# Kernel tuning notes

Measured on AMD Instinct MI355X. Metric: run time of the kernel, lower is better.

## Reference

```python
import jax, jax.numpy as jnp
import numpy as np

N = 100000          # buses
E = 200000          # branch edges (avg degree 2, power grid)
IN_DIM = 6          # x[:, 4:10]
EDGE_DIM = 4
HID = 32
OUT_DIM = 2


def _nnconv(x_in, src, dst, edge_attr, w1, b1, w2, b2, root, bias):
    """PyG NNConv (aggr='add', root_weight=True, bias=True)."""
    in_c, out_c = root.shape
    # edge-conditioned weight matrices: [E, in_c, out_c]
    h = jax.nn.relu(edge_attr @ w1 + b1)
    W = (h @ w2 + b2).reshape(-1, in_c, out_c)
    # gather source features, per-edge matvec, scatter-add to targets
    msg = jnp.einsum('ei,eio->eo', x_in[src], W)           # [E, out_c]
    agg = jax.ops.segment_sum(msg, dst, num_segments=x_in.shape[0])
    return agg + x_in @ root + bias


def setup_inputs() -> dict:
    key = jax.random.key(0)
    ks = jax.random.split(key, 8)
    inp = {
        'x': jax.random.normal(ks[0], (N, 10), dtype=jnp.float32),
        'edge_index': jax.random.randint(ks[1], (2, E), 0, N, dtype=jnp.int64),
        'edge_attr': jax.random.normal(ks[2], (E, EDGE_DIM), dtype=jnp.float32),
    }
    dims = [(IN_DIM, HID), (HID, HID), (HID, HID), (HID, OUT_DIM)]
    s = 0.1
    for i, (ic, oc) in enumerate(dims):
        k = jax.random.split(ks[3 + i], 3)
        inp[f'w1_{i}'] = jax.random.normal(k[0], (EDGE_DIM, HID), dtype=jnp.float32) * s
        inp[f'b1_{i}'] = jnp.zeros((HID,), dtype=jnp.float32)
        inp[f'w2_{i}'] = jax.random.normal(k[1], (HID, ic * oc), dtype=jnp.float32) * s
        inp[f'b2_{i}'] = jnp.zeros((ic * oc,), dtype=jnp.float32)
        inp[f'root_{i}'] = jax.random.normal(k[2], (ic, oc), dtype=jnp.float32) * s
        inp[f'bias_{i}'] = jnp.zeros((oc,), dtype=jnp.float32)
    return inp


def reference(x, edge_index, edge_attr,
              w1_0, b1_0, w2_0, b2_0, root_0, bias_0,
              w1_1, b1_1, w2_1, b2_1, root_1, bias_1,
              w1_2, b1_2, w2_2, b2_2, root_2, bias_2,
              w1_3, b1_3, w2_3, b2_3, root_3, bias_3):
    convs = [
        (w1_0, b1_0, w2_0, b2_0, root_0, bias_0),
        (w1_1, b1_1, w2_1, b2_1, root_1, bias_1),
        (w1_2, b1_2, w2_2, b2_2, root_2, bias_2),
        (w1_3, b1_3, w2_3, b2_3, root_3, bias_3),
    ]
    src, dst = edge_index[0], edge_index[1]
    h = x[:, 4:10]                                    # [N, 6]
    n_convs = len(convs)
    for i, p in enumerate(convs):
        h = _nnconv(h, src, dst, edge_attr, *p)
        if i < n_convs - 1:
            h = jax.nn.relu(h)
    return h
```

## Files before the change

### kernel.cpp

```cpp
#include <hip/hip_runtime.h>
#include <hip/hip_fp16.h>

typedef __attribute__((ext_vector_type(2)))  _Float16 half2v;
typedef __attribute__((ext_vector_type(8)))  _Float16 half8v;
typedef __attribute__((ext_vector_type(16))) float    f32x16;

static constexpr int BSWZ_STEPS = 226;
static constexpr int BSWZ_TOT   = BSWZ_STEPS * 512;
static constexpr int W1H_TOT    = 4 * 160;

struct Prm {
    const float* x;
    const float* w1[4]; const float* b1[4];
    const float* w2[4]; const float* b2[4];
    const float* root[4]; const float* bias[4];
    _Float16* xin;
    _Float16* bswz;
    _Float16* w1h;
    _Float16* aggz;
    float* outz;
    int N;
};

__global__ __launch_bounds__(256) void prep(Prm p, int NB8, int NZA, int NZO)
{
    int b = blockIdx.x;
    if (b < 452) {
        int i = b * 256 + threadIdx.x;
        int T = i >> 9, t2 = i & 511;
        int j = t2 & 7, l = (t2 >> 3) & 63;
        int g = l >> 5, o = l & 31;
        int layer, cls, t;
        if (T < 17)       { layer = 0; cls = 0; t = T; }
        else if (T < 19)  { layer = 0; cls = 1; t = T - 17; }
        else if (T < 85)  { layer = 1; cls = 0; t = T - 19; }
        else if (T < 88)  { layer = 1; cls = 1; t = T - 85; }
        else if (T < 154) { layer = 2; cls = 0; t = T - 88; }
        else if (T < 157) { layer = 2; cls = 1; t = T - 154; }
        else if (T < 223) { layer = 3; cls = 0; t = T - 157; }
        else              { layer = 3; cls = 1; t = T - 223; }
        const int INP   = (layer == 0) ? 8 : 32;
        const int IN_C  = (layer == 0) ? 6 : 32;
        const int OUT_C = (layer == 3) ? 2 : 32;
        float v = 0.f;
        if (cls == 0) {
            const int S_MAIN = 2 * INP;
            if (t < S_MAIN) {
                int kap = 16 * t + 8 * g + j;
                int k  = (INP == 8) ? (kap >> 3) : (kap >> 5);
                int ii = (INP == 8) ? (kap & 7)  : (kap & 31);
                if (ii < IN_C && o < OUT_C)
                    v = p.w2[layer][(size_t)k * (IN_C * OUT_C) + ii * OUT_C + o];
            } else {
                int ii = 16 * (t - S_MAIN) + 8 * g + j;
                if (ii < IN_C && o < OUT_C)
                    v = p.b2[layer][ii * OUT_C + o];
            }
        } else {
            const int nroot = (layer == 0) ? 1 : 2;
            if (t < nroot) {
                int ii = 16 * t + 8 * g + j;
                if (ii < IN_C && o < OUT_C)
                    v = p.root[layer][ii * OUT_C + o];
            } else {
                if (g == 0 && j == 0 && o < OUT_C)
                    v = p.bias[layer][o];
            }
        }
        p.bswz[i] = (_Float16)v;
    } else if (b < 452 + NB8) {
        int i = (b - 452) * 256 + threadIdx.x;
        if (i < p.N * 8) {
            int v = i >> 3, c = i & 7;
            float val = (c < 6) ? p.x[(size_t)v * 10 + 4 + c] : 0.f;
            p.xin[i] = (_Float16)val;
        }
    } else if (b < 452 + NB8 + NZA) {
        long long i = (long long)(b - 452 - NB8) * 256 + threadIdx.x;
        if (i < (long long)p.N * 12)
            ((uint4*)p.aggz)[i] = uint4{0u, 0u, 0u, 0u};
    } else if (b < 452 + NB8 + NZA + NZO) {
        int v = (b - 452 - NB8 - NZA) * 256 + threadIdx.x;
        if (v < p.N)
            ((float2*)p.outz)[v] = float2{0.f, 0.f};
    } else {
        for (int i = threadIdx.x; i < W1H_TOT; i += 256) {
            int layer = i / 160, r = i % 160;
            float v = (r < 128) ? p.w1[layer][r]
                                : p.b1[layer][r - 128];
            p.w1h[i] = (_Float16)v;
        }
    }
}

static __device__ __forceinline__ void gather32h(
    const _Float16* __restrict__ fprev, int s, int g, half8v& xh0, half8v& xh1)
{
    const half8v* fp = (const half8v*)(fprev + (size_t)s * 32);
    xh0 = fp[g];
    xh1 = fp[2 + g];
    #pragma unroll
    for (int j = 0; j < 8; ++j) {
        xh0[j] = xh0[j] > (_Float16)0.f ? xh0[j] : (_Float16)0.f;
        xh1[j] = xh1[j] > (_Float16)0.f ? xh1[j] : (_Float16)0.f;
    }
}

static __device__ __forceinline__ half8v splat8(_Float16 h)
{
    half8v r;
    #pragma unroll
    for (int j = 0; j < 8; ++j) r[j] = h;
    return r;
}

static __device__ __forceinline__ void pk_atomic_row(
    _Float16* __restrict__ aggH, int row, int o, float mine)
{
    float oth = __shfl_xor(mine, 1);
    if ((o & 1) == 0 && row >= 0) {
        __half2 v = __floats2half2_rn(mine, oth);
        unsafeAtomicAdd((__half2*)aggH + (((size_t)row << 5) + o) / 2, v);
    }
}

template<int INP, int OUT_C>
__global__ __launch_bounds__(1024, 8) void edge(
    const _Float16* __restrict__ xin,
    const _Float16* __restrict__ fprev,
    const int*      __restrict__ src,
    const int*      __restrict__ dst,
    const float*    __restrict__ ea,
    const _Float16* __restrict__ w1h,
    const _Float16* __restrict__ bAll,
    _Float16* __restrict__ aggH,
    float*    __restrict__ aggF,
    int E, int N, int ntileE, int ntot)
{
    constexpr int NREAL = (INP == 32) ? 66 : 17;
    constexpr int NSELF = (INP == 32) ? 3  : 2;
    constexpr int NSTEP = NREAL + NSELF;

    __shared__ half8v ldsb[NSTEP * 64];
    {
        const half8v* bp = (const half8v*)bAll;
        for (int i = threadIdx.x; i < NSTEP * 64; i += 1024)
            ldsb[i] = bp[i];
    }
    __syncthreads();

    const int lane = threadIdx.x & 63;
    const int g = lane >> 5, o = lane & 31;
    const int lrow = lane & 31;
    const int wv = (blockIdx.x * 1024 + threadIdx.x) >> 6;
    const int nw = gridDim.x * 16;

    const half2v* w1p = (const half2v*)w1h;
    const half2v* b1p = (const half2v*)(w1h + 128);
    const half2v zero2 = { (_Float16)0.f, (_Float16)0.f };

    half8v ones;
    #pragma unroll
    for (int j = 0; j < 8; ++j) ones[j] = (_Float16)0.f;
    ones[0] = (_Float16)1.f;

    for (int tile = wv; tile < ntot; tile += nw) {
        f32x16 C;
        #pragma unroll
        for (int i = 0; i < 16; ++i) C[i] = 0.f;

        if (tile < ntileE) {
            const int e0 = tile * 32;
            const int er = e0 + lrow;
            const int ec = er < E ? er : (E - 1);
            const int s  = src[ec];
            const float4 av = *(const float4*)(ea + 4ll * ec);
            half2v eax; eax[0] = (_Float16)av.x; eax[1] = eax[0];
            half2v eay; eay[0] = (_Float16)av.y; eay[1] = eay[0];
            half2v eaz; eaz[0] = (_Float16)av.z; eaz[1] = eaz[0];
            half2v eaw; eaw[0] = (_Float16)av.w; eaw[1] = eaw[0];

            half8v xh0, xh1;
            if constexpr (INP == 32) gather32h(fprev, s, g, xh0, xh1);
            else                     xh0 = *(const half8v*)(xin + (size_t)s * 8);

            if constexpr (INP == 32) {
                #pragma unroll 2
                for (int t = 0; t < 16; ++t) {
                    half2v h2 = eax * w1p[t] + b1p[t];
                    h2 = eay * w1p[16 + t] + h2;
                    h2 = eaz * w1p[32 + t] + h2;
                    h2 = eaw * w1p[48 + t] + h2;
                    h2 = __builtin_elementwise_max(h2, zero2);
                    half8v hsl = splat8(h2[0]);
                    half8v hsh = splat8(h2[1]);
                    half8v bf0 = ldsb[(4*t    ) * 64 + lane];
                    half8v bf1 = ldsb[(4*t + 1) * 64 + lane];
                    half8v bf2 = ldsb[(4*t + 2) * 64 + lane];
                    half8v bf3 = ldsb[(4*t + 3) * 64 + lane];
                    C = __builtin_amdgcn_mfma_f32_32x32x16_f16(hsl * xh0, bf0, C, 0, 0, 0);
                    C = __builtin_amdgcn_mfma_f32_32x32x16_f16(hsl * xh1, bf1, C, 0, 0, 0);
                    C = __builtin_amdgcn_mfma_f32_32x32x16_f16(hsh * xh0, bf2, C, 0, 0, 0);
                    C = __builtin_amdgcn_mfma_f32_32x32x16_f16(hsh * xh1, bf3, C, 0, 0, 0);
                }
                C = __builtin_amdgcn_mfma_f32_32x32x16_f16(xh0, ldsb[64*64 + lane], C, 0, 0, 0);
                C = __builtin_amdgcn_mfma_f32_32x32x16_f16(xh1, ldsb[65*64 + lane], C, 0, 0, 0);
            } else {
                #pragma unroll 4
                for (int t = 0; t < 16; ++t) {
                    half2v h2 = eax * w1p[t] + b1p[t];
                    h2 = eay * w1p[16 + t] + h2;
                    h2 = eaz * w1p[32 + t] + h2;
                    h2 = eaw * w1p[48 + t] + h2;
                    h2 = __builtin_elementwise_max(h2, zero2);
                    half8v hs = splat8(g ? h2[1] : h2[0]);
                    half8v bf = ldsb[t * 64 + lane];
                    C = __builtin_amdgcn_mfma_f32_32x32x16_f16(hs * xh0, bf, C, 0, 0, 0);
                }
                half8v zz;
                #pragma unroll
                for (int j = 0; j < 8; ++j) zz[j] = (_Float16)0.f;
                half8v a = (g == 0) ? xh0 : zz;
                C = __builtin_amdgcn_mfma_f32_32x32x16_f16(a, ldsb[16*64 + lane], C, 0, 0, 0);
            }

            if constexpr (OUT_C == 32) {
                #pragma unroll
                for (int q = 0; q < 4; ++q) {
                    const int eb = e0 + 8 * q + 4 * g;
                    int rows[4];
                    if (eb + 3 < E) {
                        const int4 dd = *(const int4*)(dst + eb);
                        rows[0] = dd.x; rows[1] = dd.y; rows[2] = dd.z; rows[3] = dd.w;
                    } else {
                        #pragma unroll
                        for (int m = 0; m < 4; ++m)
                            rows[m] = (eb + m < E) ? dst[eb + m] : -1;
                    }
                    #pragma unroll
                    for (int m = 0; m < 4; ++m)
                        pk_atomic_row(aggH, rows[m], o, C[4*q + m]);
                }
            } else {
                if (o < OUT_C) {
                    #pragma unroll
                    for (int q = 0; q < 4; ++q) {
                        const int eb = e0 + 8 * q + 4 * g;
                        #pragma unroll
                        for (int m = 0; m < 4; ++m)
                            if (eb + m < E)
                                unsafeAtomicAdd(aggF + (size_t)dst[eb + m] * OUT_C + o,
                                                C[4*q + m]);
                    }
                }
            }
        } else {
            const int v0 = (tile - ntileE) * 32;
            const int vr = v0 + lrow;
            const int vc = vr < N ? vr : (N - 1);

            if constexpr (INP == 32) {
                half8v xh0, xh1;
                gather32h(fprev, vc, g, xh0, xh1);
                C = __builtin_amdgcn_mfma_f32_32x32x16_f16(xh0,  ldsb[(NREAL+0)*64 + lane], C, 0, 0, 0);
                C = __builtin_amdgcn_mfma_f32_32x32x16_f16(xh1,  ldsb[(NREAL+1)*64 + lane], C, 0, 0, 0);
                C = __builtin_amdgcn_mfma_f32_32x32x16_f16(ones, ldsb[(NREAL+2)*64 + lane], C, 0, 0, 0);
            } else {
                half8v xh0 = *(const half8v*)(xin + (size_t)vc * 8);
                C = __builtin_amdgcn_mfma_f32_32x32x16_f16(xh0,  ldsb[(NREAL+0)*64 + lane], C, 0, 0, 0);
                C = __builtin_amdgcn_mfma_f32_32x32x16_f16(ones, ldsb[(NREAL+1)*64 + lane], C, 0, 0, 0);
            }

            if constexpr (OUT_C == 32) {
                #pragma unroll
                for (int q = 0; q < 4; ++q) {
                    #pragma unroll
                    for (int m = 0; m < 4; ++m) {
                        const int row = v0 + 8*q + 4*g + m;
                        pk_atomic_row(aggH, row < N ? row : -1, o, C[4*q + m]);
                    }
                }
            } else {
                if (o < OUT_C) {
                    #pragma unroll
                    for (int q = 0; q < 4; ++q) {
                        #pragma unroll
                        for (int m = 0; m < 4; ++m) {
                            const int row = v0 + 8*q + 4*g + m;
                            if (row < N)
                                unsafeAtomicAdd(aggF + (size_t)row * OUT_C + o, C[4*q + m]);
                        }
                    }
                }
            }
        }
    }
}

extern "C" void kernel_launch(void* const* d_in, const int* in_sizes, int n_in,
                              void* d_out, int out_size, void* d_ws, size_t ws_size,
                              hipStream_t stream)
{
    const float* x  = (const float*)d_in[0];
    const int*   ei = (const int*)d_in[1];
    const float* ea = (const float*)d_in[2];

    const int E = in_sizes[2] / 4;
    const int N = in_sizes[0] / 10;
    const int* src = ei;
    const int* dst = ei + E;

    const float* p[4][6];
    for (int L = 0; L < 4; ++L)
        for (int j = 0; j < 6; ++j)
            p[L][j] = (const float*)d_in[3 + 6 * L + j];

    char* w = (char*)d_ws;
    auto carve = [&](size_t bytes) {
        char* q = w; w += (bytes + 255) & ~(size_t)255; return (void*)q;
    };
    _Float16* xin  = (_Float16*)carve((size_t)N * 8 * 2);
    _Float16* aggz = (_Float16*)carve((size_t)3 * N * 32 * 2);
    _Float16* bswz = (_Float16*)carve((size_t)BSWZ_TOT * 2);
    _Float16* w1hb = (_Float16*)carve((size_t)W1H_TOT * 2);
    _Float16* agg0 = aggz;
    _Float16* agg1 = aggz + (size_t)N * 32;
    _Float16* agg2 = aggz + (size_t)2 * N * 32;
    float* out  = (float*)d_out;

    Prm prm{};
    prm.x = x;
    for (int L = 0; L < 4; ++L) {
        prm.w1[L] = p[L][0]; prm.b1[L] = p[L][1];
        prm.w2[L] = p[L][2]; prm.b2[L] = p[L][3];
        prm.root[L] = p[L][4]; prm.bias[L] = p[L][5];
    }
    prm.xin = xin; prm.bswz = bswz; prm.w1h = w1hb;
    prm.aggz = aggz; prm.outz = out; prm.N = N;

    const int NB8 = (N * 8 + 255) / 256;
    const int NZA = (N * 12 + 255) / 256;
    const int NZO = (N + 255) / 256;

    const int ntileE = (E + 31) / 32;
    const int ntileN = (N + 31) / 32;
    const int ntot   = ntileE + ntileN;
    int NB = (ntot + 15) / 16;
    if (NB > 512) NB = 512;

    prep<<<452 + NB8 + NZA + NZO + 1, 256, 0, stream>>>(prm, NB8, NZA, NZO);

    edge<8, 32><<<NB, 1024, 0, stream>>>(
        xin, nullptr, src, dst, ea, w1hb + 0 * 160,
        bswz + 0 * 512, agg0, nullptr, E, N, ntileE, ntot);

    edge<32, 32><<<NB, 1024, 0, stream>>>(
        nullptr, agg0, src, dst, ea, w1hb + 1 * 160,
        bswz + 19 * 512, agg1, nullptr, E, N, ntileE, ntot);

    edge<32, 32><<<NB, 1024, 0, stream>>>(
        nullptr, agg1, src, dst, ea, w1hb + 2 * 160,
        bswz + 88 * 512, agg2, nullptr, E, N, ntileE, ntot);

    edge<32, 2><<<NB, 1024, 0, stream>>>(
        nullptr, agg2, src, dst, ea, w1hb + 3 * 160,
        bswz + 157 * 512, nullptr, out, E, N, ntileE, ntot);
}
```

Baseline: 111.7 us.

## Replace final two-output layer MFMA path with scalar per-edge fused kernel

```diff
diff --git a/kernel.cpp b/kernel.cpp
--- a/kernel.cpp
+++ b/kernel.cpp
@@ -5,7 +5,7 @@
 typedef __attribute__((ext_vector_type(8)))  _Float16 half8v;
 typedef __attribute__((ext_vector_type(16))) float    f32x16;
 
-static constexpr int BSWZ_STEPS = 226;
+static constexpr int BSWZ_STEPS = 157;
 static constexpr int BSWZ_TOT   = BSWZ_STEPS * 512;
 static constexpr int W1H_TOT    = 4 * 160;
 
@@ -25,7 +25,7 @@
 __global__ __launch_bounds__(256) void prep(Prm p, int NB8, int NZA, int NZO)
 {
     int b = blockIdx.x;
-    if (b < 452) {
+    if (b < 314) {
         int i = b * 256 + threadIdx.x;
         int T = i >> 9, t2 = i & 511;
         int j = t2 & 7, l = (t2 >> 3) & 63;
@@ -36,12 +36,10 @@
         else if (T < 85)  { layer = 1; cls = 0; t = T - 19; }
         else if (T < 88)  { layer = 1; cls = 1; t = T - 85; }
         else if (T < 154) { layer = 2; cls = 0; t = T - 88; }
-        else if (T < 157) { layer = 2; cls = 1; t = T - 154; }
-        else if (T < 223) { layer = 3; cls = 0; t = T - 157; }
-        else              { layer = 3; cls = 1; t = T - 223; }
+        else              { layer = 2; cls = 1; t = T - 154; }
         const int INP   = (layer == 0) ? 8 : 32;
         const int IN_C  = (layer == 0) ? 6 : 32;
-        const int OUT_C = (layer == 3) ? 2 : 32;
+        const int OUT_C = 32;
         float v = 0.f;
         if (cls == 0) {
             const int S_MAIN = 2 * INP;
@@ -49,38 +47,38 @@
                 int kap = 16 * t + 8 * g + j;
                 int k  = (INP == 8) ? (kap >> 3) : (kap >> 5);
                 int ii = (INP == 8) ? (kap & 7)  : (kap & 31);
-                if (ii < IN_C && o < OUT_C)
+                if (ii < IN_C)
                     v = p.w2[layer][(size_t)k * (IN_C * OUT_C) + ii * OUT_C + o];
             } else {
                 int ii = 16 * (t - S_MAIN) + 8 * g + j;
-                if (ii < IN_C && o < OUT_C)
+                if (ii < IN_C)
                     v = p.b2[layer][ii * OUT_C + o];
             }
         } else {
             const int nroot = (layer == 0) ? 1 : 2;
             if (t < nroot) {
                 int ii = 16 * t + 8 * g + j;
-                if (ii < IN_C && o < OUT_C)
+                if (ii < IN_C)
                     v = p.root[layer][ii * OUT_C + o];
             } else {
-                if (g == 0 && j == 0 && o < OUT_C)
+                if (g == 0 && j == 0)
                     v = p.bias[layer][o];
             }
         }
         p.bswz[i] = (_Float16)v;
-    } else if (b < 452 + NB8) {
-        int i = (b - 452) * 256 + threadIdx.x;
+    } else if (b < 314 + NB8) {
+        int i = (b - 314) * 256 + threadIdx.x;
         if (i < p.N * 8) {
             int v = i >> 3, c = i & 7;
             float val = (c < 6) ? p.x[(size_t)v * 10 + 4 + c] : 0.f;
             p.xin[i] = (_Float16)val;
         }
-    } else if (b < 452 + NB8 + NZA) {
-        long long i = (long long)(b - 452 - NB8) * 256 + threadIdx.x;
+    } else if (b < 314 + NB8 + NZA) {
+        long long i = (long long)(b - 314 - NB8) * 256 + threadIdx.x;
         if (i < (long long)p.N * 12)
             ((uint4*)p.aggz)[i] = uint4{0u, 0u, 0u, 0u};
-    } else if (b < 452 + NB8 + NZA + NZO) {
-        int v = (b - 452 - NB8 - NZA) * 256 + threadIdx.x;
+    } else if (b < 314 + NB8 + NZA + NZO) {
+        int v = (b - 314 - NB8 - NZA) * 256 + threadIdx.x;
         if (v < p.N)
             ((float2*)p.outz)[v] = float2{0.f, 0.f};
     } else {
@@ -124,7 +122,7 @@
     }
 }
 
-template<int INP, int OUT_C>
+template<int INP>
 __global__ __launch_bounds__(1024, 8) void edge(
     const _Float16* __restrict__ xin,
     const _Float16* __restrict__ fprev,
@@ -134,7 +132,6 @@
     const _Float16* __restrict__ w1h,
     const _Float16* __restrict__ bAll,
     _Float16* __restrict__ aggH,
-    float*    __restrict__ aggF,
     int E, int N, int ntileE, int ntot)
 {
     constexpr int NREAL = (INP == 32) ? 66 : 17;
@@ -224,35 +221,21 @@
                 C = __builtin_amdgcn_mfma_f32_32x32x16_f16(a, ldsb[16*64 + lane], C, 0, 0, 0);
             }
 
-            if constexpr (OUT_C == 32) {
-                #pragma unroll
-                for (int q = 0; q < 4; ++q) {
-                    const int eb = e0 + 8 * q + 4 * g;
-                    int rows[4];
-                    if (eb + 3 < E) {
-                        const int4 dd = *(const int4*)(dst + eb);
-                        rows[0] = dd.x; rows[1] = dd.y; rows[2] = dd.z; rows[3] = dd.w;
-                    } else {
-                        #pragma unroll
-                        for (int m = 0; m < 4; ++m)
-                            rows[m] = (eb + m < E) ? dst[eb + m] : -1;
-                    }
+            #pragma unroll
+            for (int q = 0; q < 4; ++q) {
+                const int eb = e0 + 8 * q + 4 * g;
+                int rows[4];
+                if (eb + 3 < E) {
+                    const int4 dd = *(const int4*)(dst + eb);
+                    rows[0] = dd.x; rows[1] = dd.y; rows[2] = dd.z; rows[3] = dd.w;
+                } else {
                     #pragma unroll
                     for (int m = 0; m < 4; ++m)
-                        pk_atomic_row(aggH, rows[m], o, C[4*q + m]);
+                        rows[m] = (eb + m < E) ? dst[eb + m] : -1;
                 }
-            } else {
-                if (o < OUT_C) {
-                    #pragma unroll
-                    for (int q = 0; q < 4; ++q) {
-                        const int eb = e0 + 8 * q + 4 * g;
-                        #pragma unroll
-                        for (int m = 0; m < 4; ++m)
-                            if (eb + m < E)
-                                unsafeAtomicAdd(aggF + (size_t)dst[eb + m] * OUT_C + o,
-                                                C[4*q + m]);
-                    }
-                }
+                #pragma unroll
+                for (int m = 0; m < 4; ++m)
+                    pk_atomic_row(aggH, rows[m], o, C[4*q + m]);
             }
         } else {
             const int v0 = (tile - ntileE) * 32;
@@ -271,29 +254,101 @@
                 C = __builtin_amdgcn_mfma_f32_32x32x16_f16(ones, ldsb[(NREAL+1)*64 + lane], C, 0, 0, 0);
             }
 
-            if constexpr (OUT_C == 32) {
+            #pragma unroll
+            for (int q = 0; q < 4; ++q) {
                 #pragma unroll
-                for (int q = 0; q < 4; ++q) {
-                    #pragma unroll
-                    for (int m = 0; m < 4; ++m) {
-                        const int row = v0 + 8*q + 4*g + m;
-                        pk_atomic_row(aggH, row < N ? row : -1, o, C[4*q + m]);
-                    }
+                for (int m = 0; m < 4; ++m) {
+                    const int row = v0 + 8*q + 4*g + m;
+                    pk_atomic_row(aggH, row < N ? row : -1, o, C[4*q + m]);
                 }
-            } else {
-                if (o < OUT_C) {
-                    #pragma unroll
-                    for (int q = 0; q < 4; ++q) {
-                        #pragma unroll
-                        for (int m = 0; m < 4; ++m) {
-                            const int row = v0 + 8*q + 4*g + m;
-                            if (row < N)
-                                unsafeAtomicAdd(aggF + (size_t)row * OUT_C + o, C[4*q + m]);
-                        }
-                    }
+            }
+        }
+    }
+}
+
+__global__ __launch_bounds__(256) void l3_fused(
+    const _Float16* __restrict__ fprev,
+    const int*      __restrict__ src,
+    const int*      __restrict__ dst,
+    const float*    __restrict__ ea,
+    const _Float16* __restrict__ w1h,
+    const float*    __restrict__ w2,
+    const float*    __restrict__ b2,
+    const float*    __restrict__ root,
+    const float*    __restrict__ bias,
+    float* __restrict__ out, int E, int N)
+{
+    const int tid = blockIdx.x * 256 + threadIdx.x;
+
+    if (tid < E) {
+        const int s = src[tid], d = dst[tid];
+        const float4 av = *(const float4*)(ea + 4ll * tid);
+        half2v eax; eax[0] = (_Float16)av.x; eax[1] = eax[0];
+        half2v eay; eay[0] = (_Float16)av.y; eay[1] = eay[0];
+        half2v eaz; eaz[0] = (_Float16)av.z; eaz[1] = eaz[0];
+        half2v eaw; eaw[0] = (_Float16)av.w; eaw[1] = eaw[0];
+
+        float xf[32];
+        {
+            const half8v* fp = (const half8v*)(fprev + (size_t)s * 32);
+            #pragma unroll
+            for (int q = 0; q < 4; ++q) {
+                half8v u = fp[q];
+                #pragma unroll
+                for (int j = 0; j < 8; ++j)
+                    xf[8*q + j] = fmaxf((float)u[j], 0.f);
+            }
+        }
+
+        const half2v* w1p = (const half2v*)w1h;
+        const half2v* b1p = (const half2v*)(w1h + 128);
+        const half2v zero2 = { (_Float16)0.f, (_Float16)0.f };
+
+        float m0 = 0.f, m1 = 0.f;
+        #pragma unroll 2
+        for (int t = 0; t < 16; ++t) {
+            half2v h2 = eax * w1p[t] + b1p[t];
+            h2 = eay * w1p[16 + t] + h2;
+            h2 = eaz * w1p[32 + t] + h2;
+            h2 = eaw * w1p[48 + t] + h2;
+            h2 = __builtin_elementwise_max(h2, zero2);
+            #pragma unroll
+            for (int kk = 0; kk < 2; ++kk) {
+                const float hk = (float)h2[kk];
+                const float* wk = w2 + (size_t)(2*t + kk) * 64;
+                float s0 = 0.f, s1 = 0.f;
+                #pragma unroll
+                for (int i = 0; i < 32; ++i) {
+                    s0 = fmaf(xf[i], wk[2*i    ], s0);
+                    s1 = fmaf(xf[i], wk[2*i + 1], s1);
                 }
-            }
-        }
+                m0 = fmaf(hk, s0, m0);
+                m1 = fmaf(hk, s1, m1);
+            }
+        }
+        #pragma unroll
+        for (int i = 0; i < 32; ++i) {
+            m0 = fmaf(xf[i], b2[2*i    ], m0);
+            m1 = fmaf(xf[i], b2[2*i + 1], m1);
+        }
+        unsafeAtomicAdd(out + 2ll*d,     m0);
+        unsafeAtomicAdd(out + 2ll*d + 1, m1);
+    } else if (tid < E + N) {
+        const int v = tid - E;
+        const half8v* fp = (const half8v*)(fprev + (size_t)v * 32);
+        float a0 = bias[0], a1 = bias[1];
+        #pragma unroll
+        for (int q = 0; q < 4; ++q) {
+            half8v u = fp[q];
+            #pragma unroll
+            for (int j = 0; j < 8; ++j) {
+                float xi = fmaxf((float)u[j], 0.f);
+                a0 = fmaf(xi, root[(8*q + j) * 2    ], a0);
+                a1 = fmaf(xi, root[(8*q + j) * 2 + 1], a1);
+            }
+        }
+        unsafeAtomicAdd(out + 2ll*v,     a0);
+        unsafeAtomicAdd(out + 2ll*v + 1, a1);
     }
 }
 
@@ -348,21 +403,23 @@
     int NB = (ntot + 15) / 16;
     if (NB > 512) NB = 512;
 
-    prep<<<452 + NB8 + NZA + NZO + 1, 256, 0, stream>>>(prm, NB8, NZA, NZO);
-
-    edge<8, 32><<<NB, 1024, 0, stream>>>(
+    const int NB3 = (E + N + 255) / 256;
+
+    prep<<<314 + NB8 + NZA + NZO + 1, 256, 0, stream>>>(prm, NB8, NZA, NZO);
+
+    edge<8><<<NB, 1024, 0, stream>>>(
         xin, nullptr, src, dst, ea, w1hb + 0 * 160,
-        bswz + 0 * 512, agg0, nullptr, E, N, ntileE, ntot);
-
-    edge<32, 32><<<NB, 1024, 0, stream>>>(
+        bswz + 0 * 512, agg0, E, N, ntileE, ntot);
+
+    edge<32><<<NB, 1024, 0, stream>>>(
         nullptr, agg0, src, dst, ea, w1hb + 1 * 160,
-        bswz + 19 * 512, agg1, nullptr, E, N, ntileE, ntot);
-
-    edge<32, 32><<<NB, 1024, 0, stream>>>(
+        bswz + 19 * 512, agg1, E, N, ntileE, ntot);
+
+    edge<32><<<NB, 1024, 0, stream>>>(
         nullptr, agg1, src, dst, ea, w1hb + 2 * 160,
-        bswz + 88 * 512, agg2, nullptr, E, N, ntileE, ntot);
-
-    edge<32, 2><<<NB, 1024, 0, stream>>>(
-        nullptr, agg2, src, dst, ea, w1hb + 3 * 160,
-        bswz + 157 * 512, nullptr, out, E, N, ntileE, ntot);
-}
+        bswz + 88 * 512, agg2, E, N, ntileE, ntot);
+
+    l3_fused<<<NB3, 256, 0, stream>>>(
+        agg2, src, dst, ea, w1hb + 3 * 160,
+        p[3][2], p[3][3], p[3][4], p[3][5], out, E, N);
+}
```

Result: slower. 121.0 us (+8.3%).
